# Kernel tuning notes

Measured on AMD Instinct MI355X. Metric: run time of the kernel, lower is better.

## Reference

```python
import jax, jax.numpy as jnp
import numpy as np

N_NODES = 100000
N_EDGES = 1600000
D_IN = 128
D_OUT = 128


def setup_inputs() -> dict:
    key = jax.random.key(0)
    ks = jax.random.split(key, 7)
    x = jax.random.normal(ks[0], (N_NODES, D_IN), dtype=jnp.float32)
    edge_index = jax.random.randint(ks[1], (2, N_EDGES), 0, N_NODES, dtype=jnp.int64)
    edge_weights = jax.random.uniform(ks[2], (N_EDGES,), dtype=jnp.float32)
    s = 1.0 / np.sqrt(D_IN)
    W_lin = jax.random.uniform(ks[3], (D_IN, D_OUT), minval=-s, maxval=s, dtype=jnp.float32)
    b_lin = jax.random.uniform(ks[4], (D_OUT,), minval=-s, maxval=s, dtype=jnp.float32)
    W_agg = jax.random.uniform(ks[5], (D_IN, D_OUT), minval=-s, maxval=s, dtype=jnp.float32)
    b_agg = jax.random.uniform(ks[6], (D_OUT,), minval=-s, maxval=s, dtype=jnp.float32)
    return {"x": x, "edge_index": edge_index, "edge_weights": edge_weights,
            "W_lin": W_lin, "b_lin": b_lin, "W_agg": W_agg, "b_agg": b_agg}


def reference(x, edge_index, edge_weights, W_lin, b_lin, W_agg, b_agg):
    # self transform: [N, D_out]
    self_features = x @ W_lin + b_lin
    row, col = edge_index[0], edge_index[1]
    # gather neighbor features along edges: [E, D_in]
    neighbor_features = x[col] * edge_weights[:, None]
    # per-edge transform: [E, D_out]
    msgs = neighbor_features @ W_agg + b_agg
    # scatter-add to destination nodes (index_add_ on row)
    aggregated = jax.ops.segment_sum(msgs, row, num_segments=x.shape[0])
    return self_features + aggregated
```

## Files before the change

kernel.cpp:

```cpp
#include <hip/hip_runtime.h>

#define N_NODES 100000
#define N_EDGES 1600000
#define D 128
#define SCAN_CHUNK 1024
#define NB_SCAN ((N_NODES + SCAN_CHUNK - 1) / SCAN_CHUNK)

#define BSHIFT 9
#define BUCK_NODES 512
#define NBUCK 196
#define SCAP 10240
#define PART_CHUNK 4096
#define PART_BLOCKS ((N_EDGES + PART_CHUNK - 1) / PART_CHUNK)
#define CONV_BLOCKS 6250
#define W_BLOCKS 128

typedef __attribute__((ext_vector_type(8))) short bf16x8;
typedef __attribute__((ext_vector_type(4))) float f32x4;

__device__ __forceinline__ unsigned bf16rne(float f) {
  unsigned u = __float_as_uint(f);
  return (u + 0x7fffu + ((u >> 16) & 1u)) >> 16;
}

#define T5_OFF    200
#define T5_FRAGW  100304
#define T5_SRT    116688
#define T5_XH     3316688
#define T5_ZH     9718736
#define WS_T5_BYTES ((size_t)16120784 * 4)

#define WS_OFF   100000
#define WS_BSUM  200004
#define WS_SRT   200192
#define WS_XH    3400192
#define WS_T1_BYTES ((size_t)3400192 * 4)
#define WS_T2_BYTES ((size_t)(3400192 + 6400000) * 4)

__global__ __launch_bounds__(256) void part_kernel(
    const int* __restrict__ ei, const float* __restrict__ ew,
    const float* __restrict__ x,
    const float* __restrict__ Wl, const float* __restrict__ Wa,
    int* __restrict__ pcur, int2* __restrict__ stage,
    uint4* __restrict__ xh4, unsigned short* __restrict__ fragW) {
  __shared__ int cntL[NBUCK];
  __shared__ int gbaseL[NBUCK];
  __shared__ int curL[NBUCK];
  int bid = blockIdx.x, tid = threadIdx.x;

  if (bid < PART_BLOCKS) {
    if (tid < NBUCK) cntL[tid] = 0;
    __syncthreads();
    int e0 = bid * PART_CHUNK;
#pragma unroll
    for (int k = 0; k < PART_CHUNK / 256; k++) {
      int e = e0 + k * 256 + tid;
      if (e < N_EDGES) atomicAdd(&cntL[ei[e] >> BSHIFT], 1);
    }
    __syncthreads();
    if (tid < NBUCK) {
      gbaseL[tid] = atomicAdd(&pcur[tid], cntL[tid]);
      curL[tid] = 0;
    }
    __syncthreads();
#pragma unroll
    for (int k = 0; k < PART_CHUNK / 256; k++) {
      int e = e0 + k * 256 + tid;
      if (e < N_EDGES) {
        int d = ei[e];
        int b = d >> BSHIFT;
        int s = atomicAdd(&curL[b], 1);
        stage[(size_t)b * SCAP + gbaseL[b] + s] = make_int2(
            ei[N_EDGES + e] | ((d & (BUCK_NODES - 1)) << 17), __float_as_int(ew[e]));
      }
    }
  } else if (bid < PART_BLOCKS + CONV_BLOCKS) {
    int g = (bid - PART_BLOCKS) * 256 + tid;
    const float4* xp = reinterpret_cast<const float4*>(x);
    float4 a = xp[(size_t)g * 2];
    float4 b = xp[(size_t)g * 2 + 1];
    uint4 o;
    o.x = bf16rne(a.x) | (bf16rne(a.y) << 16);
    o.y = bf16rne(a.z) | (bf16rne(a.w) << 16);
    o.z = bf16rne(b.x) | (bf16rne(b.y) << 16);
    o.w = bf16rne(b.z) | (bf16rne(b.w) << 16);
    xh4[g] = o;
  } else {
    int tau = (bid - PART_BLOCKS - CONV_BLOCKS) * 256 + tid;
    int slot = tau >> 3, j = tau & 7;
    int lane = slot & 63, ft = slot >> 6;
    int t = ft & 7, s = ft >> 3;
    int kl = (s & 3) * 32 + (lane >> 4) * 8 + j;
    int n = t * 16 + (lane & 15);
    float v = (s < 4 ? Wl : Wa)[kl * 128 + n];
    fragW[slot * 8 + j] = (unsigned short)bf16rne(v);
  }
}

__global__ __launch_bounds__(256) void binB2_kernel(const int* __restrict__ pcur,
                                                    const int2* __restrict__ stage,
                                                    int* __restrict__ off,
                                                    int2* __restrict__ srt) {
  __shared__ int pc[NBUCK];
  __shared__ int sa[BUCK_NODES];
  __shared__ int sb[BUCK_NODES];
  __shared__ int curL[BUCK_NODES];
  __shared__ int baseS, mS;
  int b = blockIdx.x, tid = threadIdx.x;
  if (tid < NBUCK) pc[tid] = pcur[tid];
  for (int i = tid; i < BUCK_NODES; i += 256) sa[i] = 0;
  __syncthreads();
  if (tid == 0) {
    int s = 0;
    for (int i = 0; i < b; i++) s += pc[i];
    baseS = s;
    mS = pc[b];
  }
  __syncthreads();
  int base = baseS, m = mS;
  const int2* sp = stage + (size_t)b * SCAP;
  for (int r = tid; r < m; r += 256)
    atomicAdd(&sa[((unsigned)sp[r].x) >> 17], 1);
  __syncthreads();
  int* srcb = sa;
  int* dstb = sb;
  for (int o = 1; o < BUCK_NODES; o <<= 1) {
    for (int p = tid; p < BUCK_NODES; p += 256)
      dstb[p] = srcb[p] + (p >= o ? srcb[p - o] : 0);
    __syncthreads();
    int* t = srcb; srcb = dstb; dstb = t;
  }
  int nb = b << BSHIFT;
  int nn = min(BUCK_NODES, N_NODES - nb);
  for (int i = tid; i < BUCK_NODES; i += 256) {
    int ex = i ? srcb[i - 1] : 0;
    curL[i] = ex;
    if (i < nn) off[nb + i] = base + ex;
  }
  if (tid == 0 && b == NBUCK - 1) off[N_NODES] = base + srcb[nn - 1];
  __syncthreads();
  for (int r = tid; r < m; r += 256) {
    int2 rec = sp[r];
    int ldst = ((unsigned)rec.x) >> 17;
    int s = atomicAdd(&curL[ldst], 1);
    srt[base + s] = make_int2(rec.x & 0x1FFFF, rec.y);
  }
}

__global__ __launch_bounds__(256) void gather_zh_kernel(const unsigned* __restrict__ xh,
                                                        const int* __restrict__ off,
                                                        const int2* __restrict__ srt,
                                                        unsigned* __restrict__ zh) {
  int gid = blockIdx.x * 256 + threadIdx.x;
  int n = gid >> 5;
  int lane = gid & 31;
  int beg = off[n], end = off[n + 1];
  float4 acc = make_float4(0.f, 0.f, 0.f, 0.f);
  int e = beg;
  for (; e + 3 < end; e += 4) {
    int2 r0 = srt[e];
    int2 r1 = srt[e + 1];
    int2 r2 = srt[e + 2];
    int2 r3 = srt[e + 3];
    uint2 p0 = *reinterpret_cast<const uint2*>(xh + (size_t)r0.x * 64 + lane * 2);
    uint2 p1 = *reinterpret_cast<const uint2*>(xh + (size_t)r1.x * 64 + lane * 2);
    uint2 p2 = *reinterpret_cast<const uint2*>(xh + (size_t)r2.x * 64 + lane * 2);
    uint2 p3 = *reinterpret_cast<const uint2*>(xh + (size_t)r3.x * 64 + lane * 2);
    float w0 = __int_as_float(r0.y), w1 = __int_as_float(r1.y);
    float w2 = __int_as_float(r2.y), w3 = __int_as_float(r3.y);
    acc.x = fmaf(w0, __uint_as_float(p0.x << 16), acc.x);
    acc.y = fmaf(w0, __uint_as_float(p0.x & 0xffff0000u), acc.y);
    acc.z = fmaf(w0, __uint_as_float(p0.y << 16), acc.z);
    acc.w = fmaf(w0, __uint_as_float(p0.y & 0xffff0000u), acc.w);
    acc.x = fmaf(w1, __uint_as_float(p1.x << 16), acc.x);
    acc.y = fmaf(w1, __uint_as_float(p1.x & 0xffff0000u), acc.y);
    acc.z = fmaf(w1, __uint_as_float(p1.y << 16), acc.z);
    acc.w = fmaf(w1, __uint_as_float(p1.y & 0xffff0000u), acc.w);
    acc.x = fmaf(w2, __uint_as_float(p2.x << 16), acc.x);
    acc.y = fmaf(w2, __uint_as_float(p2.x & 0xffff0000u), acc.y);
    acc.z = fmaf(w2, __uint_as_float(p2.y << 16), acc.z);
    acc.w = fmaf(w2, __uint_as_float(p2.y & 0xffff0000u), acc.w);
    acc.x = fmaf(w3, __uint_as_float(p3.x << 16), acc.x);
    acc.y = fmaf(w3, __uint_as_float(p3.x & 0xffff0000u), acc.y);
    acc.z = fmaf(w3, __uint_as_float(p3.y << 16), acc.z);
    acc.w = fmaf(w3, __uint_as_float(p3.y & 0xffff0000u), acc.w);
  }
  for (; e < end; e++) {
    int2 r0 = srt[e];
    uint2 p0 = *reinterpret_cast<const uint2*>(xh + (size_t)r0.x * 64 + lane * 2);
    float w0 = __int_as_float(r0.y);
    acc.x = fmaf(w0, __uint_as_float(p0.x << 16), acc.x);
    acc.y = fmaf(w0, __uint_as_float(p0.x & 0xffff0000u), acc.y);
    acc.z = fmaf(w0, __uint_as_float(p0.y << 16), acc.z);
    acc.w = fmaf(w0, __uint_as_float(p0.y & 0xffff0000u), acc.w);
  }
  uint2 o;
  o.x = bf16rne(acc.x) | (bf16rne(acc.y) << 16);
  o.y = bf16rne(acc.z) | (bf16rne(acc.w) << 16);
  *reinterpret_cast<uint2*>(zh + (size_t)n * 64 + lane * 2) = o;
}

__global__ __launch_bounds__(256) void mfma_gemm_kernel(
    const short* __restrict__ xh, const short* __restrict__ zh,
    const short* __restrict__ fragW, const int* __restrict__ off,
    const float* __restrict__ bl, const float* __restrict__ ba,
    float* __restrict__ out) {
  int tid = threadIdx.x;
  int wave = tid >> 6, lane = tid & 63;
  int m = lane & 15, q = lane >> 4;
  int R = blockIdx.x * 64 + wave * 16;
  const short* xrow = xh + (size_t)(R + m) * D + q * 8;
  const short* zrow = zh + (size_t)(R + m) * D + q * 8;
  const short* fw = fragW + (size_t)lane * 8;

  f32x4 acc[8];
#pragma unroll
  for (int t = 0; t < 8; t++) acc[t] = (f32x4){0.f, 0.f, 0.f, 0.f};

#pragma unroll
  for (int s = 0; s < 8; s++) {
    bf16x8 a = *reinterpret_cast<const bf16x8*>(s < 4 ? xrow + s * 32
                                                      : zrow + (s - 4) * 32);
#pragma unroll
    for (int t = 0; t < 8; t++) {
      bf16x8 b = *reinterpret_cast<const bf16x8*>(fw + (size_t)((s * 8 + t) * 64) * 8);
      acc[t] = __builtin_amdgcn_mfma_f32_16x16x32_bf16(a, b, acc[t], 0, 0, 0);
    }
  }

  float blv[8], bav[8];
#pragma unroll
  for (int t = 0; t < 8; t++) {
    blv[t] = bl[t * 16 + m];
    bav[t] = ba[t * 16 + m];
  }
#pragma unroll
  for (int r = 0; r < 4; r++) {
    int row = R + q * 4 + r;
    if (row < N_NODES) {
      float dg = (float)(off[row + 1] - off[row]);
#pragma unroll
      for (int t = 0; t < 8; t++)
        out[(size_t)row * D + t * 16 + m] = acc[t][r] + blv[t] + dg * bav[t];
    }
  }
}


__global__ __launch_bounds__(256) void hist_kernel(const int* __restrict__ ei,
                                                   int* __restrict__ cnt) {
  int e = blockIdx.x * 256 + threadIdx.x;
  if (e < N_EDGES) atomicAdd(&cnt[ei[e]], 1);
}

__global__ __launch_bounds__(256) void block_sum_kernel(const int* __restrict__ cnt,
                                                        int* __restrict__ bsum) {
  int base = blockIdx.x * SCAN_CHUNK;
  int s = 0;
#pragma unroll
  for (int k = 0; k < 4; k++) {
    int i = base + (int)threadIdx.x + k * 256;
    if (i < N_NODES) s += cnt[i];
  }
  __shared__ int red[4];
  for (int o = 32; o > 0; o >>= 1) s += __shfl_down(s, o, 64);
  if ((threadIdx.x & 63) == 0) red[threadIdx.x >> 6] = s;
  __syncthreads();
  if (threadIdx.x == 0) bsum[blockIdx.x] = red[0] + red[1] + red[2] + red[3];
}

__global__ __launch_bounds__(128) void scan_bsum_kernel(int* __restrict__ bsum,
                                                        int* __restrict__ off) {
  __shared__ int sh[128];
  int t = threadIdx.x;
  int v = (t < NB_SCAN) ? bsum[t] : 0;
  sh[t] = v;
  __syncthreads();
  for (int o = 1; o < 128; o <<= 1) {
    int add = (t >= o) ? sh[t - o] : 0;
    __syncthreads();
    sh[t] += add;
    __syncthreads();
  }
  if (t < NB_SCAN) bsum[t] = sh[t] - v;
  if (t == 0) off[N_NODES] = sh[127];
}

__global__ __launch_bounds__(256) void scan_offsets_kernel(const int* __restrict__ cnt,
                                                           const int* __restrict__ bsum,
                                                           int* __restrict__ off) {
  __shared__ int sh[256];
  int t = threadIdx.x;
  int i0 = blockIdx.x * SCAN_CHUNK + t * 4;
  int c[4];
#pragma unroll
  for (int k = 0; k < 4; k++) c[k] = (i0 + k < N_NODES) ? cnt[i0 + k] : 0;
  int ls = c[0] + c[1] + c[2] + c[3];
  sh[t] = ls;
  __syncthreads();
  for (int o = 1; o < 256; o <<= 1) {
    int add = (t >= o) ? sh[t - o] : 0;
    __syncthreads();
    sh[t] += add;
    __syncthreads();
  }
  int run = bsum[blockIdx.x] + sh[t] - ls;
#pragma unroll
  for (int k = 0; k < 4; k++) {
    if (i0 + k < N_NODES) off[i0 + k] = run;
    run += c[k];
  }
}

__global__ __launch_bounds__(256) void fill_kernel(const int* __restrict__ ei,
                                                   const float* __restrict__ ew,
                                                   const int* __restrict__ off,
                                                   int* __restrict__ cur,
                                                   int2* __restrict__ srt) {
  int e = blockIdx.x * 256 + threadIdx.x;
  if (e >= N_EDGES) return;
  int dst = ei[e];
  int p = off[dst] + atomicAdd(&cur[dst], 1);
  srt[p] = make_int2(ei[N_EDGES + e], __float_as_int(ew[e]));
}

__global__ __launch_bounds__(256) void convert_kernel(const float* __restrict__ x,
                                                      uint4* __restrict__ xh) {
  int i = blockIdx.x * 256 + threadIdx.x;
  const float4* xp = reinterpret_cast<const float4*>(x);
  float4 a = xp[(size_t)i * 2];
  float4 b = xp[(size_t)i * 2 + 1];
  uint4 o;
  o.x = bf16rne(a.x) | (bf16rne(a.y) << 16);
  o.y = bf16rne(a.z) | (bf16rne(a.w) << 16);
  o.z = bf16rne(b.x) | (bf16rne(b.y) << 16);
  o.w = bf16rne(b.z) | (bf16rne(b.w) << 16);
  xh[i] = o;
}

__global__ __launch_bounds__(256) void gather_bf16_kernel(const unsigned* __restrict__ xh,
                                                          const int* __restrict__ off,
                                                          const int2* __restrict__ srt,
                                                          float* __restrict__ z,
                                                          float* __restrict__ degf) {
  int gid = blockIdx.x * 256 + threadIdx.x;
  int n = gid >> 5;
  int lane = gid & 31;
  if (n >= N_NODES) return;
  int beg = off[n], end = off[n + 1];
  float4 acc = make_float4(0.f, 0.f, 0.f, 0.f);
  int e = beg;
  for (; e + 1 < end; e += 2) {
    int2 r0 = srt[e];
    int2 r1 = srt[e + 1];
    uint2 p0 = *reinterpret_cast<const uint2*>(xh + (size_t)r0.x * 64 + lane * 2);
    uint2 p1 = *reinterpret_cast<const uint2*>(xh + (size_t)r1.x * 64 + lane * 2);
    float w0 = __int_as_float(r0.y);
    float w1 = __int_as_float(r1.y);
    acc.x = fmaf(w0, __uint_as_float(p0.x << 16), acc.x);
    acc.y = fmaf(w0, __uint_as_float(p0.x & 0xffff0000u), acc.y);
    acc.z = fmaf(w0, __uint_as_float(p0.y << 16), acc.z);
    acc.w = fmaf(w0, __uint_as_float(p0.y & 0xffff0000u), acc.w);
    acc.x = fmaf(w1, __uint_as_float(p1.x << 16), acc.x);
    acc.y = fmaf(w1, __uint_as_float(p1.x & 0xffff0000u), acc.y);
    acc.z = fmaf(w1, __uint_as_float(p1.y << 16), acc.z);
    acc.w = fmaf(w1, __uint_as_float(p1.y & 0xffff0000u), acc.w);
  }
  if (e < end) {
    int2 r0 = srt[e];
    uint2 p0 = *reinterpret_cast<const uint2*>(xh + (size_t)r0.x * 64 + lane * 2);
    float w0 = __int_as_float(r0.y);
    acc.x = fmaf(w0, __uint_as_float(p0.x << 16), acc.x);
    acc.y = fmaf(w0, __uint_as_float(p0.x & 0xffff0000u), acc.y);
    acc.z = fmaf(w0, __uint_as_float(p0.y << 16), acc.z);
    acc.w = fmaf(w0, __uint_as_float(p0.y & 0xffff0000u), acc.w);
  }
  *reinterpret_cast<float4*>(z + (size_t)n * D + (lane << 2)) = acc;
  if (lane == 0) degf[n] = (float)(end - beg);
}

__global__ __launch_bounds__(256) void gather_f32_kernel(const float* __restrict__ x,
                                                         const int* __restrict__ off,
                                                         const int2* __restrict__ srt,
                                                         float* __restrict__ z,
                                                         float* __restrict__ degf) {
  int gid = blockIdx.x * 256 + threadIdx.x;
  int n = gid >> 5;
  int lane = gid & 31;
  if (n >= N_NODES) return;
  int beg = off[n], end = off[n + 1];
  float4 acc = make_float4(0.f, 0.f, 0.f, 0.f);
  for (int e = beg; e < end; e++) {
    int2 r0 = srt[e];
    float4 x0 = *reinterpret_cast<const float4*>(x + (size_t)r0.x * D + (lane << 2));
    float w0 = __int_as_float(r0.y);
    acc.x = fmaf(w0, x0.x, acc.x); acc.y = fmaf(w0, x0.y, acc.y);
    acc.z = fmaf(w0, x0.z, acc.z); acc.w = fmaf(w0, x0.w, acc.w);
  }
  *reinterpret_cast<float4*>(z + (size_t)n * D + (lane << 2)) = acc;
  if (lane == 0) degf[n] = (float)(end - beg);
}

__global__ __launch_bounds__(256) void scatter_kernel(const float* __restrict__ x,
                                                      const int* __restrict__ ei,
                                                      const float* __restrict__ ew,
                                                      float* __restrict__ z,
                                                      float* __restrict__ deg) {
  long long g = (long long)blockIdx.x * 256 + threadIdx.x;
  int e = (int)(g >> 5);
  int lane = (int)(g & 31);
  if (e >= N_EDGES) return;
  int dst = ei[e];
  int src = ei[N_EDGES + e];
  float w = ew[e];
  float4 xv = *reinterpret_cast<const float4*>(x + (size_t)src * D + (lane << 2));
  float* o = z + (size_t)dst * D + (lane << 2);
  atomicAdd(o + 0, w * xv.x);
  atomicAdd(o + 1, w * xv.y);
  atomicAdd(o + 2, w * xv.z);
  atomicAdd(o + 3, w * xv.w);
  if (lane == 0) atomicAdd(deg + dst, 1.0f);
}

__global__ __launch_bounds__(256) void fused_gemm_kernel(const float* __restrict__ x,
                                                         const float* __restrict__ Wl,
                                                         const float* __restrict__ bl,
                                                         const float* __restrict__ Wa,
                                                         const float* __restrict__ ba,
                                                         const float* __restrict__ deg,
                                                         float* __restrict__ out) {
  __shared__ float xs[32 * 16];
  __shared__ float zs[32 * 16];
  __shared__ float wls[16 * 128];
  __shared__ float was[16 * 128];
  const int tid = threadIdx.x;
  const int row0 = blockIdx.x * 32;
  const int c4 = tid & 31;
  const int r0 = tid >> 5;
  float4 acc[4];
#pragma unroll
  for (int i = 0; i < 4; i++) acc[i] = make_float4(0.f, 0.f, 0.f, 0.f);

  for (int k0 = 0; k0 < D; k0 += 16) {
    {
      int t = tid & 127;
      int r = t >> 2;
      int kc = (t & 3) << 2;
      const float* sp = (tid < 128) ? x : out;
      float* dp = (tid < 128) ? xs : zs;
      *reinterpret_cast<float4*>(dp + r * 16 + kc) =
          *reinterpret_cast<const float4*>(sp + (size_t)(row0 + r) * D + k0 + kc);
    }
#pragma unroll
    for (int i = 0; i < 2; i++) {
      int f = tid + i * 256;
      int kk = f >> 5;
      int cc = (f & 31) << 2;
      *reinterpret_cast<float4*>(wls + kk * 128 + cc) =
          *reinterpret_cast<const float4*>(Wl + (size_t)(k0 + kk) * D + cc);
      *reinterpret_cast<float4*>(was + kk * 128 + cc) =
          *reinterpret_cast<const float4*>(Wa + (size_t)(k0 + kk) * D + cc);
    }
    __syncthreads();
#pragma unroll
    for (int kk = 0; kk < 16; kk++) {
      float4 wl = *reinterpret_cast<const float4*>(wls + kk * 128 + (c4 << 2));
      float4 wa = *reinterpret_cast<const float4*>(was + kk * 128 + (c4 << 2));
#pragma unroll
      for (int rr = 0; rr < 4; rr++) {
        int r2 = r0 + rr * 8;
        float xv = xs[r2 * 16 + kk];
        float zv = zs[r2 * 16 + kk];
        acc[rr].x = fmaf(xv, wl.x, fmaf(zv, wa.x, acc[rr].x));
        acc[rr].y = fmaf(xv, wl.y, fmaf(zv, wa.y, acc[rr].y));
        acc[rr].z = fmaf(xv, wl.z, fmaf(zv, wa.z, acc[rr].z));
        acc[rr].w = fmaf(xv, wl.w, fmaf(zv, wa.w, acc[rr].w));
      }
    }
    __syncthreads();
  }

  float4 blv = *reinterpret_cast<const float4*>(bl + (c4 << 2));
  float4 bav = *reinterpret_cast<const float4*>(ba + (c4 << 2));
#pragma unroll
  for (int rr = 0; rr < 4; rr++) {
    int r = row0 + r0 + rr * 8;
    float d = deg[r];
    float4 o;
    o.x = acc[rr].x + blv.x + d * bav.x;
    o.y = acc[rr].y + blv.y + d * bav.y;
    o.z = acc[rr].z + blv.z + d * bav.z;
    o.w = acc[rr].w + blv.w + d * bav.w;
    *reinterpret_cast<float4*>(out + (size_t)r * D + (c4 << 2)) = o;
  }
}

extern "C" void kernel_launch(void* const* d_in, const int* in_sizes, int n_in,
                              void* d_out, int out_size, void* d_ws, size_t ws_size,
                              hipStream_t stream) {
  const float* x  = (const float*)d_in[0];
  const int*   ei = (const int*)d_in[1];
  const float* ew = (const float*)d_in[2];
  const float* Wl = (const float*)d_in[3];
  const float* bl = (const float*)d_in[4];
  const float* Wa = (const float*)d_in[5];
  const float* ba = (const float*)d_in[6];
  float* out = (float*)d_out;

  if (ws_size >= WS_T5_BYTES) {
    int* pcur = (int*)d_ws;
    int* off = pcur + T5_OFF;
    unsigned short* fragW = (unsigned short*)(pcur + T5_FRAGW);
    int2* srt = (int2*)(pcur + T5_SRT);
    unsigned* xh = (unsigned*)(pcur + T5_XH);
    unsigned* zh = (unsigned*)(pcur + T5_ZH);
    int2* stage = (int2*)(pcur + T5_ZH);

    hipMemsetAsync(pcur, 0, NBUCK * sizeof(int), stream);
    part_kernel<<<PART_BLOCKS + CONV_BLOCKS + W_BLOCKS, 256, 0, stream>>>(
        ei, ew, x, Wl, Wa, pcur, stage, (uint4*)xh, fragW);
    binB2_kernel<<<NBUCK, 256, 0, stream>>>(pcur, stage, off, srt);
    gather_zh_kernel<<<N_NODES * 32 / 256, 256, 0, stream>>>(xh, off, srt, zh);
    mfma_gemm_kernel<<<1563, 256, 0, stream>>>((const short*)xh, (const short*)zh,
                                               (const short*)fragW, off, bl, ba, out);
  } else if (ws_size >= WS_T1_BYTES) {
    int*  cnt  = (int*)d_ws;
    int*  off  = cnt + WS_OFF;
    int*  bsum = cnt + WS_BSUM;
    int2* srt  = (int2*)(cnt + WS_SRT);
    float* degf = (float*)cnt;

    hipMemsetAsync(cnt, 0, (size_t)N_NODES * sizeof(int), stream);
    hist_kernel<<<(N_EDGES + 255) / 256, 256, 0, stream>>>(ei, cnt);
    block_sum_kernel<<<NB_SCAN, 256, 0, stream>>>(cnt, bsum);
    scan_bsum_kernel<<<1, 128, 0, stream>>>(bsum, off);
    scan_offsets_kernel<<<NB_SCAN, 256, 0, stream>>>(cnt, bsum, off);
    hipMemsetAsync(cnt, 0, (size_t)N_NODES * sizeof(int), stream);
    fill_kernel<<<(N_EDGES + 255) / 256, 256, 0, stream>>>(ei, ew, off, cnt, srt);

    if (ws_size >= WS_T2_BYTES) {
      unsigned* xh = (unsigned*)(cnt + WS_XH);
      convert_kernel<<<(N_NODES * D / 8) / 256, 256, 0, stream>>>(x, (uint4*)xh);
      gather_bf16_kernel<<<(N_NODES * 32 + 255) / 256, 256, 0, stream>>>(xh, off, srt, out, degf);
    } else {
      gather_f32_kernel<<<(N_NODES * 32 + 255) / 256, 256, 0, stream>>>(x, off, srt, out, degf);
    }
    fused_gemm_kernel<<<N_NODES / 32, 256, 0, stream>>>(x, Wl, bl, Wa, ba, degf, out);
  } else {
    float* deg = (float*)d_ws;
    hipMemsetAsync(out, 0, (size_t)N_NODES * D * sizeof(float), stream);
    hipMemsetAsync(deg, 0, (size_t)N_NODES * sizeof(float), stream);
    scatter_kernel<<<(N_EDGES * 32) / 256, 256, 0, stream>>>(x, ei, ew, out, deg);
    fused_gemm_kernel<<<N_NODES / 32, 256, 0, stream>>>(x, Wl, bl, Wa, ba, deg, out);
  }
}
```

Baseline: 284.4 us.

## Split bf16 features into 16-dim slices for cache-local neighbor gather

Stores the bf16 copy of x and the aggregated z as 8 column slices of 16 dims each (32 bytes per row), so each gather block works on one slice whose whole table (about 3.2 MB) can stay cache-resident. The gather kernel now uses 4 threads per node per slice and visits slices in interleaved block order, and the GEMM A-operand addressing is updated to match. Edge records are read and z is written with nontemporal hints so they do not evict the slice from cache. In exchange, every node's edge list is read 8 times and each random access fetches only 8 bytes per lane, so sector efficiency may drop.

```diff
diff --git a/kernel.cpp b/kernel.cpp
--- a/kernel.cpp
+++ b/kernel.cpp
@@ -14,6 +14,13 @@
 #define PART_BLOCKS ((N_EDGES + PART_CHUNK - 1) / PART_CHUNK)
 #define CONV_BLOCKS 6250
 #define W_BLOCKS 128
+
+#define NSLICE 8
+#define SLICE_DIMS 16
+#define SLICE_ROWS 100032
+#define SLICE_SH ((size_t)SLICE_ROWS * SLICE_DIMS)
+#define SLICE_U4 (SLICE_SH / 8)
+#define GATHER_NG 1563
 
 typedef __attribute__((ext_vector_type(8))) short bf16x8;
 typedef __attribute__((ext_vector_type(4))) float f32x4;
@@ -76,6 +83,8 @@
     }
   } else if (bid < PART_BLOCKS + CONV_BLOCKS) {
     int g = (bid - PART_BLOCKS) * 256 + tid;
+    int n = g >> 4;
+    int j = g & 15;
     const float4* xp = reinterpret_cast<const float4*>(x);
     float4 a = xp[(size_t)g * 2];
     float4 b = xp[(size_t)g * 2 + 1];
@@ -84,7 +93,7 @@
     o.y = bf16rne(a.z) | (bf16rne(a.w) << 16);
     o.z = bf16rne(b.x) | (bf16rne(b.y) << 16);
     o.w = bf16rne(b.z) | (bf16rne(b.w) << 16);
-    xh4[g] = o;
+    xh4[(size_t)(j >> 1) * SLICE_U4 + (size_t)n * 2 + (j & 1)] = o;
   } else {
     int tau = (bid - PART_BLOCKS - CONV_BLOCKS) * 256 + tid;
     int slot = tau >> 3, j = tau & 7;
@@ -147,27 +156,29 @@
   }
 }
 
-__global__ __launch_bounds__(256) void gather_zh_kernel(const unsigned* __restrict__ xh,
+__global__ __launch_bounds__(256) void gather_zh_kernel(const unsigned short* __restrict__ xh,
                                                         const int* __restrict__ off,
                                                         const int2* __restrict__ srt,
-                                                        unsigned* __restrict__ zh) {
-  int gid = blockIdx.x * 256 + threadIdx.x;
-  int n = gid >> 5;
-  int lane = gid & 31;
-  int beg = off[n], end = off[n + 1];
+                                                        unsigned short* __restrict__ zh) {
+  int slice = blockIdx.x & 7;
+  int nb = (blockIdx.x >> 3) * 64 + ((int)threadIdx.x >> 2);
+  int lane = threadIdx.x & 3;
+  if (nb >= N_NODES) return;
+  const unsigned short* xsl = xh + (size_t)slice * SLICE_SH + lane * 4;
+  int beg = off[nb], end = off[nb + 1];
   float4 acc = make_float4(0.f, 0.f, 0.f, 0.f);
   int e = beg;
   for (; e + 3 < end; e += 4) {
-    int2 r0 = srt[e];
-    int2 r1 = srt[e + 1];
-    int2 r2 = srt[e + 2];
-    int2 r3 = srt[e + 3];
-    uint2 p0 = *reinterpret_cast<const uint2*>(xh + (size_t)r0.x * 64 + lane * 2);
-    uint2 p1 = *reinterpret_cast<const uint2*>(xh + (size_t)r1.x * 64 + lane * 2);
-    uint2 p2 = *reinterpret_cast<const uint2*>(xh + (size_t)r2.x * 64 + lane * 2);
-    uint2 p3 = *reinterpret_cast<const uint2*>(xh + (size_t)r3.x * 64 + lane * 2);
-    float w0 = __int_as_float(r0.y), w1 = __int_as_float(r1.y);
-    float w2 = __int_as_float(r2.y), w3 = __int_as_float(r3.y);
+    long long q0 = __builtin_nontemporal_load(reinterpret_cast<const long long*>(srt + e));
+    long long q1 = __builtin_nontemporal_load(reinterpret_cast<const long long*>(srt + e + 1));
+    long long q2 = __builtin_nontemporal_load(reinterpret_cast<const long long*>(srt + e + 2));
+    long long q3 = __builtin_nontemporal_load(reinterpret_cast<const long long*>(srt + e + 3));
+    uint2 p0 = *reinterpret_cast<const uint2*>(xsl + (size_t)(unsigned)(q0 & 0xffffffff) * 16);
+    uint2 p1 = *reinterpret_cast<const uint2*>(xsl + (size_t)(unsigned)(q1 & 0xffffffff) * 16);
+    uint2 p2 = *reinterpret_cast<const uint2*>(xsl + (size_t)(unsigned)(q2 & 0xffffffff) * 16);
+    uint2 p3 = *reinterpret_cast<const uint2*>(xsl + (size_t)(unsigned)(q3 & 0xffffffff) * 16);
+    float w0 = __int_as_float((int)(q0 >> 32)), w1 = __int_as_float((int)(q1 >> 32));
+    float w2 = __int_as_float((int)(q2 >> 32)), w3 = __int_as_float((int)(q3 >> 32));
     acc.x = fmaf(w0, __uint_as_float(p0.x << 16), acc.x);
     acc.y = fmaf(w0, __uint_as_float(p0.x & 0xffff0000u), acc.y);
     acc.z = fmaf(w0, __uint_as_float(p0.y << 16), acc.z);
@@ -186,18 +197,20 @@
     acc.w = fmaf(w3, __uint_as_float(p3.y & 0xffff0000u), acc.w);
   }
   for (; e < end; e++) {
-    int2 r0 = srt[e];
-    uint2 p0 = *reinterpret_cast<const uint2*>(xh + (size_t)r0.x * 64 + lane * 2);
-    float w0 = __int_as_float(r0.y);
+    long long q0 = __builtin_nontemporal_load(reinterpret_cast<const long long*>(srt + e));
+    uint2 p0 = *reinterpret_cast<const uint2*>(xsl + (size_t)(unsigned)(q0 & 0xffffffff) * 16);
+    float w0 = __int_as_float((int)(q0 >> 32));
     acc.x = fmaf(w0, __uint_as_float(p0.x << 16), acc.x);
     acc.y = fmaf(w0, __uint_as_float(p0.x & 0xffff0000u), acc.y);
     acc.z = fmaf(w0, __uint_as_float(p0.y << 16), acc.z);
     acc.w = fmaf(w0, __uint_as_float(p0.y & 0xffff0000u), acc.w);
   }
-  uint2 o;
-  o.x = bf16rne(acc.x) | (bf16rne(acc.y) << 16);
-  o.y = bf16rne(acc.z) | (bf16rne(acc.w) << 16);
-  *reinterpret_cast<uint2*>(zh + (size_t)n * 64 + lane * 2) = o;
+  unsigned lo = bf16rne(acc.x) | (bf16rne(acc.y) << 16);
+  unsigned hi = bf16rne(acc.z) | (bf16rne(acc.w) << 16);
+  unsigned long long v = (unsigned long long)lo | ((unsigned long long)hi << 32);
+  __builtin_nontemporal_store(
+      v, reinterpret_cast<unsigned long long*>(zh + (size_t)slice * SLICE_SH +
+                                               (size_t)nb * 16 + lane * 4));
 }
 
 __global__ __launch_bounds__(256) void mfma_gemm_kernel(
@@ -209,8 +222,9 @@
   int wave = tid >> 6, lane = tid & 63;
   int m = lane & 15, q = lane >> 4;
   int R = blockIdx.x * 64 + wave * 16;
-  const short* xrow = xh + (size_t)(R + m) * D + q * 8;
-  const short* zrow = zh + (size_t)(R + m) * D + q * 8;
+  size_t rbase = (size_t)(R + m) * 16 + (size_t)(q & 1) * 8 + (size_t)(q >> 1) * SLICE_SH;
+  const short* xb = xh + rbase;
+  const short* zb = zh + rbase;
   const short* fw = fragW + (size_t)lane * 8;
 
   f32x4 acc[8];
@@ -219,8 +233,8 @@
 
 #pragma unroll
   for (int s = 0; s < 8; s++) {
-    bf16x8 a = *reinterpret_cast<const bf16x8*>(s < 4 ? xrow + s * 32
-                                                      : zrow + (s - 4) * 32);
+    const short* ap = (s < 4 ? xb : zb) + (size_t)(s & 3) * (2 * SLICE_SH);
+    bf16x8 a = *reinterpret_cast<const bf16x8*>(ap);
 #pragma unroll
     for (int t = 0; t < 8; t++) {
       bf16x8 b = *reinterpret_cast<const bf16x8*>(fw + (size_t)((s * 8 + t) * 64) * 8);
@@ -512,15 +526,15 @@
     int* off = pcur + T5_OFF;
     unsigned short* fragW = (unsigned short*)(pcur + T5_FRAGW);
     int2* srt = (int2*)(pcur + T5_SRT);
-    unsigned* xh = (unsigned*)(pcur + T5_XH);
-    unsigned* zh = (unsigned*)(pcur + T5_ZH);
+    unsigned short* xh = (unsigned short*)(pcur + T5_XH);
+    unsigned short* zh = (unsigned short*)(pcur + T5_ZH);
     int2* stage = (int2*)(pcur + T5_ZH);
 
     hipMemsetAsync(pcur, 0, NBUCK * sizeof(int), stream);
     part_kernel<<<PART_BLOCKS + CONV_BLOCKS + W_BLOCKS, 256, 0, stream>>>(
         ei, ew, x, Wl, Wa, pcur, stage, (uint4*)xh, fragW);
     binB2_kernel<<<NBUCK, 256, 0, stream>>>(pcur, stage, off, srt);
-    gather_zh_kernel<<<N_NODES * 32 / 256, 256, 0, stream>>>(xh, off, srt, zh);
+    gather_zh_kernel<<<GATHER_NG * NSLICE, 256, 0, stream>>>(xh, off, srt, zh);
     mfma_gemm_kernel<<<1563, 256, 0, stream>>>((const short*)xh, (const short*)zh,
                                                (const short*)fragW, off, bl, ba, out);
   } else if (ws_size >= WS_T1_BYTES) {
```

Measured after the change: 386.3 us. 35.8% more time.
